# Optimization experiments

Hardware: AMD Instinct MI355X
Metric: run time of the kernel (lower is better)

## Reference

```python
import jax, jax.numpy as jnp
import numpy as np

EPS = 1e-5  # BatchNorm1d default eps


def _gcn_layer(x, src, dst, ew, W, b, N):
    # PyG GCNConv: h = x @ W, add self-loops (weight 1), symmetric norm, aggregate at dst, + bias
    h = x @ W
    loop = jnp.arange(N)
    src_a = jnp.concatenate([src, loop])
    dst_a = jnp.concatenate([dst, loop])
    ew_a = jnp.concatenate([ew, jnp.ones((N,), x.dtype)])
    deg = jax.ops.segment_sum(ew_a, dst_a, num_segments=N)  # [N]
    dinv = jax.lax.rsqrt(deg)  # deg >= 1 thanks to self-loops
    norm = dinv[src_a] * ew_a * dinv[dst_a]  # [E+N]
    out = jax.ops.segment_sum(h[src_a] * norm[:, None], dst_a, num_segments=N)
    return out + b


def _bn_relu(h, gamma, beta):
    # training-mode BatchNorm1d over the node dimension (biased variance)
    mean = h.mean(axis=0)
    var = jnp.mean((h - mean) ** 2, axis=0)
    return jax.nn.relu((h - mean) * jax.lax.rsqrt(var + EPS) * gamma + beta)


def setup_inputs() -> dict:
    key = jax.random.key(0)
    ks = jax.random.split(key, 8)
    N, E, D, H = 100000, 1600000, 64, 64
    x = jax.random.normal(ks[0], (N, D), dtype=jnp.float32)
    edge_index = jax.random.randint(ks[1], (2, E), 0, N, dtype=jnp.int64)
    edge_weight = jax.random.uniform(ks[2], (E,), dtype=jnp.float32)
    s = 1.0 / np.sqrt(D)
    W1 = jax.random.uniform(ks[3], (D, H), jnp.float32, -s, s)
    b1 = jnp.zeros((H,), jnp.float32)
    gamma1 = jnp.ones((H,), jnp.float32)
    beta1 = jnp.zeros((H,), jnp.float32)
    s2 = 1.0 / np.sqrt(H)
    W2 = jax.random.uniform(ks[4], (H, H), jnp.float32, -s2, s2)
    b2 = jnp.zeros((H,), jnp.float32)
    gamma2 = jnp.ones((H,), jnp.float32)
    beta2 = jnp.zeros((H,), jnp.float32)
    return {"x": x, "edge_index": edge_index, "edge_weight": edge_weight,
            "W1": W1, "b1": b1, "gamma1": gamma1, "beta1": beta1,
            "W2": W2, "b2": b2, "gamma2": gamma2, "beta2": beta2}


def reference(x, edge_index, edge_weight, W1, b1, gamma1, beta1, W2, b2, gamma2, beta2):
    N = x.shape[0]
    src, dst = edge_index[0], edge_index[1]  # messages flow src -> dst
    h = _gcn_layer(x, src, dst, edge_weight, W1, b1, N)
    h = _bn_relu(h, gamma1, beta1)
    h = _gcn_layer(h, src, dst, edge_weight, W2, b2, N)
    h = _bn_relu(h, gamma2, beta2)
    return h
```

## Files before the change

kernel.cpp:

```cpp
#include <hip/hip_runtime.h>
#include <hip/hip_fp16.h>


#define NPB   200
#define NBMAX 512
#define CAP   5120
#define CHUNK 8192

typedef unsigned long long u64;
typedef unsigned int u32;
typedef u32 u32x4 __attribute__((ext_vector_type(4)));

__global__ __launch_bounds__(512) void k_init(int* gcur, float* stats) {
  int t = threadIdx.x;
  if (t < NBMAX) gcur[t] = 0;
  if (t < 256) stats[t] = 0.f;
}

__global__ __launch_bounds__(256) void k_bucket(const int* __restrict__ ei,
                                                const float* __restrict__ ew,
                                                int* gcur, u64* __restrict__ bkt,
                                                int E, int NB) {
  __shared__ int lcnt[NBMAX];
  __shared__ int lbase[NBMAX];
  int t = threadIdx.x;
  for (int b = t; b < NBMAX; b += 256) lcnt[b] = 0;
  __syncthreads();
  int lo = blockIdx.x * CHUNK;
  int hi = min(lo + CHUNK, E);
  for (int i = lo + t; i < hi; i += 256)
    atomicAdd(&lcnt[ei[E + i] / NPB], 1);
  __syncthreads();
  for (int b = t; b < NB; b += 256) {
    int c = lcnt[b];
    lbase[b] = c ? atomicAdd(&gcur[b], c) : 0;
    lcnt[b] = 0;
  }
  __syncthreads();
  for (int i = lo + t; i < hi; i += 256) {
    int src = ei[i], dst = ei[E + i];
    float w = ew[i];
    int b = dst / NPB;
    int pos = lbase[b] + atomicAdd(&lcnt[b], 1);
    if (pos < CAP) {
      unsigned wq = (unsigned)(w * 1073741824.0f);
      if (wq > 0x3FFFFFFFu) wq = 0x3FFFFFFFu;
      bkt[(size_t)b * CAP + pos] =
          ((u64)(unsigned)dst << 47) | ((u64)(unsigned)src << 30) | (u64)wq;
    }
  }
}

__global__ __launch_bounds__(256) void k_sort(const u64* __restrict__ bkt,
                                              const int* __restrict__ gcur,
                                              u32* __restrict__ csr,
                                              int2* __restrict__ row,
                                              float* __restrict__ dinv, int N) {
  __shared__ u64 sorted[CAP];
  __shared__ int hist[256];
  __shared__ int offs[256];
  __shared__ int cur[NPB];
  __shared__ int cpArr[NPB];
  __shared__ float dv[NPB];
  int b = blockIdx.x, t = threadIdx.x;
  for (int i = t; i < CAP; i += 256) sorted[i] = 0ULL;
  hist[t] = 0;
  if (t < NPB) cur[t] = 0;
  __syncthreads();
  int cnt = min(gcur[b], CAP);
  size_t base = (size_t)b * CAP;
  for (int i = t; i < cnt; i += 256) {
    int dl = (int)(bkt[base + i] >> 47) - b * NPB;
    atomicAdd(&hist[dl], 1);
  }
  __syncthreads();
  int c = (t < NPB) ? ((hist[t] + 7) & ~7) : 0;
  offs[t] = c;
  __syncthreads();
  for (int o = 1; o < 256; o <<= 1) {
    int x = (t >= o) ? offs[t - o] : 0;
    __syncthreads();
    offs[t] += x;
    __syncthreads();
  }
  int total = offs[255];
  int myoff = offs[t] - c;
  __syncthreads();
  offs[t] = myoff;
  if (t < NPB) cpArr[t] = c;
  __syncthreads();
  for (int i = t; i < cnt; i += 256) {
    u64 u = bkt[base + i];
    int dl = (int)(u >> 47) - b * NPB;
    int pos = offs[dl] + atomicAdd(&cur[dl], 1);
    if (pos < CAP) sorted[pos] = u;
  }
  __syncthreads();
  for (int q = t; q < NPB * 4; q += 256) {
    int n = q >> 2, s = q & 3;
    int o = offs[n], cp = cpArr[n];
    float sum = 0.f;
    for (int j = o + s; j < o + cp; j += 4)
      sum += (float)(unsigned)(sorted[j] & 0x3FFFFFFFu);
    sum += __shfl_xor(sum, 1);
    sum += __shfl_xor(sum, 2);
    if (s == 0) {
      float d = rsqrtf(sum * (1.0f / 1073741824.0f) + 1.0f);
      dv[n] = d;
      int gn = b * NPB + n;
      if (gn < N) dinv[gn] = d;
    }
  }
  __syncthreads();
  int totalC = min(total, CAP);
  for (int j = t; j < totalC; j += 256) {
    u64 u = sorted[j];
    unsigned wq = (unsigned)(u & 0x3FFFFFFFu);
    int dl = (int)(u >> 47) - b * NPB;
    int dlc = (wq == 0) ? 0 : dl;
    float w = (float)wq * (1.0f / 1073741824.0f) * dv[dlc];
    unsigned q15 = (unsigned)(w * 32768.0f + 0.5f);
    if (q15 > 32767u) q15 = 32767u;
    unsigned s = (unsigned)((u >> 30) & 0x1FFFFu);
    csr[base + j] = (s << 15) | q15;
  }
  for (int n = t; n < NPB; n += 256) {
    int gn = b * NPB + n;
    if (gn < N) {
      int o = offs[n];
      int cp = min(cpArr[n], max(0, CAP - o)) & ~7;
      row[gn] = make_int2((int)(base + o), cp);
    }
  }
}

__global__ __launch_bounds__(256) void k_fold(u32* __restrict__ csr,
                                              const float* __restrict__ dinv,
                                              int total4, int N) {
  int i = blockIdx.x * 256 + threadIdx.x;
  if (i >= total4) return;
  uint4 q = ((uint4*)csr)[i];
#pragma unroll
  for (int k = 0; k < 4; ++k) {
    u32 u = (&q.x)[k];
    int s = (int)(u >> 15);
    float d = dinv[min(s, N - 1)];
    unsigned nq = (unsigned)((float)(u & 0x7FFFu) * d + 0.5f);
    (&q.x)[k] = (u & 0xFFFF8000u) | nq;
  }
  ((uint4*)csr)[i] = q;
}

__device__ inline unsigned pk2(float a, float b) {
  __half2 h = __floats2half2_rn(a, b);
  return *reinterpret_cast<unsigned*>(&h);
}

template <int FUSE>
__global__ __launch_bounds__(256) void k_gemm(const float* __restrict__ X,
                                              const float* __restrict__ W,
                                              __half* __restrict__ Y, int N,
                                              const float* __restrict__ scale,
                                              const float* __restrict__ shift) {
  __shared__ float Wl[64 * 64];
  __shared__ float sc[64], sh[64];
  int tid = threadIdx.x;
  {
    float4* Wl4 = (float4*)Wl;
    const float4* W4 = (const float4*)W;
#pragma unroll
    for (int i = 0; i < 4; ++i) Wl4[tid + i * 256] = W4[tid + i * 256];
  }
  if (FUSE && tid < 64) { sc[tid] = scale[tid]; sh[tid] = shift[tid]; }
  __syncthreads();
  int row = blockIdx.x * 64 + (tid >> 2);
  if (row >= N) return;
  int c0 = (tid & 3) * 16;
  float4 a0 = make_float4(0.f, 0.f, 0.f, 0.f), a1 = a0, a2 = a0, a3 = a0;
  const float4* Xr = (const float4*)(X + (size_t)row * 64);
#pragma unroll
  for (int kk = 0; kk < 16; ++kk) {
    float4 xv = Xr[kk];
    if (FUSE) {
      int k4 = kk * 4;
      xv.x = fmaxf(fmaf(xv.x, sc[k4 + 0], sh[k4 + 0]), 0.f);
      xv.y = fmaxf(fmaf(xv.y, sc[k4 + 1], sh[k4 + 1]), 0.f);
      xv.z = fmaxf(fmaf(xv.z, sc[k4 + 2], sh[k4 + 2]), 0.f);
      xv.w = fmaxf(fmaf(xv.w, sc[k4 + 3], sh[k4 + 3]), 0.f);
    }
    const float* wbase = &Wl[(kk * 4) * 64 + c0];
#pragma unroll
    for (int d = 0; d < 4; ++d) {
      float xk = (d == 0) ? xv.x : (d == 1) ? xv.y : (d == 2) ? xv.z : xv.w;
      const float4* Wr = (const float4*)(wbase + d * 64);
      float4 w0 = Wr[0], w1 = Wr[1], w2 = Wr[2], w3 = Wr[3];
      a0.x = fmaf(xk, w0.x, a0.x); a0.y = fmaf(xk, w0.y, a0.y);
      a0.z = fmaf(xk, w0.z, a0.z); a0.w = fmaf(xk, w0.w, a0.w);
      a1.x = fmaf(xk, w1.x, a1.x); a1.y = fmaf(xk, w1.y, a1.y);
      a1.z = fmaf(xk, w1.z, a1.z); a1.w = fmaf(xk, w1.w, a1.w);
      a2.x = fmaf(xk, w2.x, a2.x); a2.y = fmaf(xk, w2.y, a2.y);
      a2.z = fmaf(xk, w2.z, a2.z); a2.w = fmaf(xk, w2.w, a2.w);
      a3.x = fmaf(xk, w3.x, a3.x); a3.y = fmaf(xk, w3.y, a3.y);
      a3.z = fmaf(xk, w3.z, a3.z); a3.w = fmaf(xk, w3.w, a3.w);
    }
  }
  uint4 p0, p1;
  p0.x = pk2(a0.x, a0.y); p0.y = pk2(a0.z, a0.w);
  p0.z = pk2(a1.x, a1.y); p0.w = pk2(a1.z, a1.w);
  p1.x = pk2(a2.x, a2.y); p1.y = pk2(a2.z, a2.w);
  p1.z = pk2(a3.x, a3.y); p1.w = pk2(a3.z, a3.w);
  uint4* Y4 = (uint4*)(Y + (size_t)row * 64 + c0);
  Y4[0] = p0; Y4[1] = p1;
}

__global__ __launch_bounds__(256) void k_agg(const __half* __restrict__ H,
                                             const int2* __restrict__ row,
                                             const u32* __restrict__ csr,
                                             const float* __restrict__ dinv,
                                             const float* __restrict__ bias,
                                             float* __restrict__ out,
                                             float* __restrict__ sums,
                                             float* __restrict__ sumsq, int N) {
  const float QS = 1.0f / 32768.0f;
  int lane = threadIdx.x & 63;
  int wib = threadIdx.x >> 6;
  int wid = blockIdx.x * 4 + wib;
  int nw = gridDim.x * 4;
  float b = bias[lane];
  float ssum = 0.f, ssq = 0.f;
  for (int n = wid; n < N; n += nw) {
    int2 r = row[n];
    const u32x4* c4 = (const u32x4*)(csr + r.x);
    int cntp = r.y;
    float di = dinv[n];
    float hn = __half2float(H[(size_t)n * 64 + lane]);
    float acc0 = 0.f, acc1 = 0.f, acc2 = 0.f, acc3 = 0.f;
    for (int j = 0; j < cntp; j += 8) {
      u32x4 qa = __builtin_nontemporal_load(&c4[(j >> 2) + 0]);
      u32x4 qb = __builtin_nontemporal_load(&c4[(j >> 2) + 1]);
      int s0 = (int)(qa.x >> 15), s1 = (int)(qa.y >> 15);
      int s2 = (int)(qa.z >> 15), s3 = (int)(qa.w >> 15);
      int s4 = (int)(qb.x >> 15), s5 = (int)(qb.y >> 15);
      int s6 = (int)(qb.z >> 15), s7 = (int)(qb.w >> 15);
      float w0 = (float)(qa.x & 0x7FFFu) * QS, w1 = (float)(qa.y & 0x7FFFu) * QS;
      float w2 = (float)(qa.z & 0x7FFFu) * QS, w3 = (float)(qa.w & 0x7FFFu) * QS;
      float w4 = (float)(qb.x & 0x7FFFu) * QS, w5 = (float)(qb.y & 0x7FFFu) * QS;
      float w6 = (float)(qb.z & 0x7FFFu) * QS, w7 = (float)(qb.w & 0x7FFFu) * QS;
      float h0 = __half2float(H[(size_t)s0 * 64 + lane]);
      float h1 = __half2float(H[(size_t)s1 * 64 + lane]);
      float h2 = __half2float(H[(size_t)s2 * 64 + lane]);
      float h3 = __half2float(H[(size_t)s3 * 64 + lane]);
      float h4 = __half2float(H[(size_t)s4 * 64 + lane]);
      float h5 = __half2float(H[(size_t)s5 * 64 + lane]);
      float h6 = __half2float(H[(size_t)s6 * 64 + lane]);
      float h7 = __half2float(H[(size_t)s7 * 64 + lane]);
      acc0 = fmaf(w0, h0, acc0); acc1 = fmaf(w1, h1, acc1);
      acc2 = fmaf(w2, h2, acc2); acc3 = fmaf(w3, h3, acc3);
      acc0 = fmaf(w4, h4, acc0); acc1 = fmaf(w5, h5, acc1);
      acc2 = fmaf(w6, h6, acc2); acc3 = fmaf(w7, h7, acc3);
    }
    float v = (acc0 + acc1) + (acc2 + acc3) + di * di * hn + b;
    __builtin_nontemporal_store(v, &out[(size_t)n * 64 + lane]);
    ssum += v;
    ssq = fmaf(v, v, ssq);
  }
  __shared__ float ls[4][64];
  __shared__ float ls2[4][64];
  ls[wib][lane] = ssum; ls2[wib][lane] = ssq;
  __syncthreads();
  if (wib == 0) {
    float a = ls[0][lane] + ls[1][lane] + ls[2][lane] + ls[3][lane];
    float c = ls2[0][lane] + ls2[1][lane] + ls2[2][lane] + ls2[3][lane];
    atomicAdd(&sums[lane], a);
    atomicAdd(&sumsq[lane], c);
  }
}

__global__ __launch_bounds__(64) void k_finalize(const float* __restrict__ sums,
                                                 const float* __restrict__ sumsq,
                                                 const float* __restrict__ gamma,
                                                 const float* __restrict__ beta,
                                                 float* __restrict__ scale,
                                                 float* __restrict__ shift, float invN) {
  int t = threadIdx.x;
  if (t < 64) {
    float mean = sums[t] * invN;
    float var = sumsq[t] * invN - mean * mean;
    float sc = gamma[t] * rsqrtf(var + 1e-5f);
    scale[t] = sc;
    shift[t] = fmaf(-mean, sc, beta[t]);
  }
}

__global__ __launch_bounds__(256) void k_bnrelu(float* __restrict__ Y,
                                                const float* __restrict__ scale,
                                                const float* __restrict__ shift, int n4) {
  int i = blockIdx.x * 256 + threadIdx.x;
  if (i >= n4) return;
  float4 v = ((float4*)Y)[i];
  int f = (i & 15) * 4;
  v.x = fmaxf(fmaf(v.x, scale[f + 0], shift[f + 0]), 0.f);
  v.y = fmaxf(fmaf(v.y, scale[f + 1], shift[f + 1]), 0.f);
  v.z = fmaxf(fmaf(v.z, scale[f + 2], shift[f + 2]), 0.f);
  v.w = fmaxf(fmaf(v.w, scale[f + 3], shift[f + 3]), 0.f);
  ((float4*)Y)[i] = v;
}

extern "C" void kernel_launch(void* const* d_in, const int* in_sizes, int n_in,
                              void* d_out, int out_size, void* d_ws, size_t ws_size,
                              hipStream_t stream) {
  const float* x   = (const float*)d_in[0];
  const int*   ei  = (const int*)d_in[1];
  const float* ew  = (const float*)d_in[2];
  const float* W1  = (const float*)d_in[3];
  const float* b1  = (const float*)d_in[4];
  const float* g1  = (const float*)d_in[5];
  const float* be1 = (const float*)d_in[6];
  const float* W2  = (const float*)d_in[7];
  const float* b2  = (const float*)d_in[8];
  const float* g2  = (const float*)d_in[9];
  const float* be2 = (const float*)d_in[10];
  int N = in_sizes[0] / 64;
  int E = in_sizes[1] / 2;
  float* out = (float*)d_out;

  int NB = (N + NPB - 1) / NPB;

  char* ws = (char*)d_ws;
  size_t off = 0;
  auto alloc = [&](size_t bytes) {
    char* p = ws + off;
    off = (off + bytes + 255) & ~(size_t)255;
    return p;
  };

  int*    gcur  = (int*)alloc(NBMAX * 4);
  float*  dinv  = (float*)alloc((size_t)N * 4);
  __half* h1    = (__half*)alloc((size_t)N * 64 * 2);
  float*  stats = (float*)alloc(256 * 4);
  float*  scsh  = (float*)alloc(256 * 4);
  int2*   row   = (int2*)alloc((size_t)N * 8);
  u64*    bkt   = (u64*)alloc((size_t)NB * CAP * 8);
  u32*    csr   = (u32*)alloc((size_t)NB * CAP * 4);

  float *sums1 = stats, *sumsq1 = stats + 64, *sums2 = stats + 128, *sumsq2 = stats + 192;
  float *scale1 = scsh, *shift1 = scsh + 64, *scale2 = scsh + 128, *shift2 = scsh + 192;

  int total4 = NB * CAP / 4;

  k_init<<<1, 512, 0, stream>>>(gcur, stats);
  k_bucket<<<(E + CHUNK - 1) / CHUNK, 256, 0, stream>>>(ei, ew, gcur, bkt, E, NB);
  k_sort<<<NB, 256, 0, stream>>>(bkt, gcur, csr, row, dinv, N);
  k_fold<<<(total4 + 255) / 256, 256, 0, stream>>>(csr, dinv, total4, N);

  k_gemm<0><<<(N + 63) / 64, 256, 0, stream>>>(x, W1, h1, N, nullptr, nullptr);
  k_agg<<<2048, 256, 0, stream>>>(h1, row, csr, dinv, b1, out, sums1, sumsq1, N);
  k_finalize<<<1, 64, 0, stream>>>(sums1, sumsq1, g1, be1, scale1, shift1, 1.0f / N);

  k_gemm<1><<<(N + 63) / 64, 256, 0, stream>>>(out, W2, h1, N, scale1, shift1);
  k_agg<<<2048, 256, 0, stream>>>(h1, row, csr, dinv, b2, out, sums2, sumsq2, N);
  k_finalize<<<1, 64, 0, stream>>>(sums2, sumsq2, g2, be2, scale2, shift2, 1.0f / N);
  k_bnrelu<<<(N * 16 + 255) / 256, 256, 0, stream>>>(out, scale2, shift2, N * 16);
}
```

Before: 302.2 us.

## Split wave into two half-waves each gathering half2 features per edge

The aggregation kernel now has each 64-lane wave process two edges at once: lanes 0-31 and 32-63 each take alternating edges, and each lane loads a __half2 (two features) instead of a single half. The two half-wave partial sums are combined with a cross-lane shuffle before the store, and only the lower half writes output and stats. The aim is wider per-lane gather loads and fewer serial iterations per node. The grid size is also doubled. The cost is the extra shuffle and half-idle lanes at the epilogue.

Result: slower. 377.2 us (+24.8%).

```diff
diff --git a/kernel.cpp b/kernel.cpp
--- a/kernel.cpp
+++ b/kernel.cpp
@@ -10,6 +10,7 @@
 typedef unsigned long long u64;
 typedef unsigned int u32;
 typedef u32 u32x4 __attribute__((ext_vector_type(4)));
+typedef float f32x2 __attribute__((ext_vector_type(2)));
 
 __global__ __launch_bounds__(512) void k_init(int* gcur, float* stats) {
   int t = threadIdx.x;
@@ -222,51 +223,67 @@
                                              float* __restrict__ sums,
                                              float* __restrict__ sumsq, int N) {
   const float QS = 1.0f / 32768.0f;
+  const __half2* H2 = (const __half2*)H;
   int lane = threadIdx.x & 63;
   int wib = threadIdx.x >> 6;
+  int fp = lane & 31;
+  int hi = lane >> 5;
+  int f0 = fp * 2;
   int wid = blockIdx.x * 4 + wib;
   int nw = gridDim.x * 4;
-  float b = bias[lane];
-  float ssum = 0.f, ssq = 0.f;
+  float b0 = bias[f0], b1 = bias[f0 + 1];
+  float ssum0 = 0.f, ssq0 = 0.f, ssum1 = 0.f, ssq1 = 0.f;
   for (int n = wid; n < N; n += nw) {
     int2 r = row[n];
     const u32x4* c4 = (const u32x4*)(csr + r.x);
     int cntp = r.y;
     float di = dinv[n];
-    float hn = __half2float(H[(size_t)n * 64 + lane]);
-    float acc0 = 0.f, acc1 = 0.f, acc2 = 0.f, acc3 = 0.f;
+    float2 a0 = make_float2(0.f, 0.f), a1 = a0, a2 = a0, a3 = a0;
     for (int j = 0; j < cntp; j += 8) {
       u32x4 qa = __builtin_nontemporal_load(&c4[(j >> 2) + 0]);
       u32x4 qb = __builtin_nontemporal_load(&c4[(j >> 2) + 1]);
-      int s0 = (int)(qa.x >> 15), s1 = (int)(qa.y >> 15);
-      int s2 = (int)(qa.z >> 15), s3 = (int)(qa.w >> 15);
-      int s4 = (int)(qb.x >> 15), s5 = (int)(qb.y >> 15);
-      int s6 = (int)(qb.z >> 15), s7 = (int)(qb.w >> 15);
-      float w0 = (float)(qa.x & 0x7FFFu) * QS, w1 = (float)(qa.y & 0x7FFFu) * QS;
-      float w2 = (float)(qa.z & 0x7FFFu) * QS, w3 = (float)(qa.w & 0x7FFFu) * QS;
-      float w4 = (float)(qb.x & 0x7FFFu) * QS, w5 = (float)(qb.y & 0x7FFFu) * QS;
-      float w6 = (float)(qb.z & 0x7FFFu) * QS, w7 = (float)(qb.w & 0x7FFFu) * QS;
-      float h0 = __half2float(H[(size_t)s0 * 64 + lane]);
-      float h1 = __half2float(H[(size_t)s1 * 64 + lane]);
-      float h2 = __half2float(H[(size_t)s2 * 64 + lane]);
-      float h3 = __half2float(H[(size_t)s3 * 64 + lane]);
-      float h4 = __half2float(H[(size_t)s4 * 64 + lane]);
-      float h5 = __half2float(H[(size_t)s5 * 64 + lane]);
-      float h6 = __half2float(H[(size_t)s6 * 64 + lane]);
-      float h7 = __half2float(H[(size_t)s7 * 64 + lane]);
-      acc0 = fmaf(w0, h0, acc0); acc1 = fmaf(w1, h1, acc1);
-      acc2 = fmaf(w2, h2, acc2); acc3 = fmaf(w3, h3, acc3);
-      acc0 = fmaf(w4, h4, acc0); acc1 = fmaf(w5, h5, acc1);
-      acc2 = fmaf(w6, h6, acc2); acc3 = fmaf(w7, h7, acc3);
-    }
-    float v = (acc0 + acc1) + (acc2 + acc3) + di * di * hn + b;
-    __builtin_nontemporal_store(v, &out[(size_t)n * 64 + lane]);
-    ssum += v;
-    ssq = fmaf(v, v, ssq);
+      u32 e0 = hi ? qa.y : qa.x;
+      u32 e1 = hi ? qa.w : qa.z;
+      u32 e2 = hi ? qb.y : qb.x;
+      u32 e3 = hi ? qb.w : qb.z;
+      int s0 = (int)(e0 >> 15), s1 = (int)(e1 >> 15);
+      int s2 = (int)(e2 >> 15), s3 = (int)(e3 >> 15);
+      float w0 = (float)(e0 & 0x7FFFu) * QS;
+      float w1 = (float)(e1 & 0x7FFFu) * QS;
+      float w2 = (float)(e2 & 0x7FFFu) * QS;
+      float w3 = (float)(e3 & 0x7FFFu) * QS;
+      __half2 h0 = H2[(size_t)s0 * 32 + fp];
+      __half2 h1 = H2[(size_t)s1 * 32 + fp];
+      __half2 h2 = H2[(size_t)s2 * 32 + fp];
+      __half2 h3 = H2[(size_t)s3 * 32 + fp];
+      float2 g0 = __half22float2(h0), g1 = __half22float2(h1);
+      float2 g2 = __half22float2(h2), g3 = __half22float2(h3);
+      a0.x = fmaf(w0, g0.x, a0.x); a0.y = fmaf(w0, g0.y, a0.y);
+      a1.x = fmaf(w1, g1.x, a1.x); a1.y = fmaf(w1, g1.y, a1.y);
+      a2.x = fmaf(w2, g2.x, a2.x); a2.y = fmaf(w2, g2.y, a2.y);
+      a3.x = fmaf(w3, g3.x, a3.x); a3.y = fmaf(w3, g3.y, a3.y);
+    }
+    float ax = (a0.x + a1.x) + (a2.x + a3.x);
+    float ay = (a0.y + a1.y) + (a2.y + a3.y);
+    ax += __shfl_xor(ax, 32);
+    ay += __shfl_xor(ay, 32);
+    float2 hn = __half22float2(H2[(size_t)n * 32 + fp]);
+    float d2 = di * di;
+    float vx = ax + d2 * hn.x + b0;
+    float vy = ay + d2 * hn.y + b1;
+    if (lane < 32) {
+      f32x2 v2; v2.x = vx; v2.y = vy;
+      __builtin_nontemporal_store(v2, (f32x2*)&out[(size_t)n * 64 + f0]);
+    }
+    ssum0 += vx; ssq0 = fmaf(vx, vx, ssq0);
+    ssum1 += vy; ssq1 = fmaf(vy, vy, ssq1);
   }
   __shared__ float ls[4][64];
   __shared__ float ls2[4][64];
-  ls[wib][lane] = ssum; ls2[wib][lane] = ssq;
+  if (lane < 32) {
+    ls[wib][f0] = ssum0;  ls[wib][f0 + 1] = ssum1;
+    ls2[wib][f0] = ssq0;  ls2[wib][f0 + 1] = ssq1;
+  }
   __syncthreads();
   if (wib == 0) {
     float a = ls[0][lane] + ls[1][lane] + ls[2][lane] + ls[3][lane];
@@ -354,11 +371,11 @@
   k_fold<<<(total4 + 255) / 256, 256, 0, stream>>>(csr, dinv, total4, N);
 
   k_gemm<0><<<(N + 63) / 64, 256, 0, stream>>>(x, W1, h1, N, nullptr, nullptr);
-  k_agg<<<2048, 256, 0, stream>>>(h1, row, csr, dinv, b1, out, sums1, sumsq1, N);
+  k_agg<<<4096, 256, 0, stream>>>(h1, row, csr, dinv, b1, out, sums1, sumsq1, N);
   k_finalize<<<1, 64, 0, stream>>>(sums1, sumsq1, g1, be1, scale1, shift1, 1.0f / N);
 
   k_gemm<1><<<(N + 63) / 64, 256, 0, stream>>>(out, W2, h1, N, scale1, shift1);
-  k_agg<<<2048, 256, 0, stream>>>(h1, row, csr, dinv, b2, out, sums2, sumsq2, N);
+  k_agg<<<4096, 256, 0, stream>>>(h1, row, csr, dinv, b2, out, sums2, sumsq2, N);
   k_finalize<<<1, 64, 0, stream>>>(sums2, sumsq2, g2, be2, scale2, shift2, 1.0f / N);
   k_bnrelu<<<(N * 16 + 255) / 256, 256, 0, stream>>>(out, scale2, shift2, N * 16);
 }
```

## Compute degrees in separate pass, fold src norm into sort, fuse BN finalize

Applied to the files above, without the earlier changes.

Adds a k_deg kernel that computes dinv per bucket with integer shared atomics. This lets k_sort apply both the src and dst normalisation directly and drops the separate k_fold pass over the CSR. The BN finalize kernels are folded into the consumers (the second gemm and bnrelu), removing two tiny launches. The aggregation loop is unrolled to 16 edges per iteration with rows padded to multiples of 16, and CAP grows to fit the extra padding. The larger padding adds zero-weight work and raises shared memory use in k_sort, and the fixed-point integer degree sum loses some precision.

Measured after the change: 298.6 us. About the same (-1.2%).

```diff
diff --git a/kernel.cpp b/kernel.cpp
--- a/kernel.cpp
+++ b/kernel.cpp
@@ -4,7 +4,7 @@
 
 #define NPB   200
 #define NBMAX 512
-#define CAP   5120
+#define CAP   6144
 #define CHUNK 8192
 
 typedef unsigned long long u64;
@@ -51,11 +51,33 @@
   }
 }
 
+__global__ __launch_bounds__(256) void k_deg(const u64* __restrict__ bkt,
+                                             const int* __restrict__ gcur,
+                                             float* __restrict__ dinv, int N) {
+  __shared__ int dq[NPB];
+  int b = blockIdx.x, t = threadIdx.x;
+  for (int n = t; n < NPB; n += 256) dq[n] = 0;
+  __syncthreads();
+  int cnt = min(gcur[b], CAP);
+  size_t base = (size_t)b * CAP;
+  for (int i = t; i < cnt; i += 256) {
+    u64 u = bkt[base + i];
+    int dl = (int)(u >> 47) - b * NPB;
+    atomicAdd(&dq[dl], (int)((unsigned)(u & 0x3FFFFFFFu) >> 6));
+  }
+  __syncthreads();
+  for (int n = t; n < NPB; n += 256) {
+    int gn = b * NPB + n;
+    if (gn < N)
+      dinv[gn] = rsqrtf((float)dq[n] * (1.0f / 16777216.0f) + 1.0f);
+  }
+}
+
 __global__ __launch_bounds__(256) void k_sort(const u64* __restrict__ bkt,
                                               const int* __restrict__ gcur,
+                                              const float* __restrict__ dinv,
                                               u32* __restrict__ csr,
-                                              int2* __restrict__ row,
-                                              float* __restrict__ dinv, int N) {
+                                              int2* __restrict__ row, int N) {
   __shared__ u64 sorted[CAP];
   __shared__ int hist[256];
   __shared__ int offs[256];
@@ -65,7 +87,11 @@
   int b = blockIdx.x, t = threadIdx.x;
   for (int i = t; i < CAP; i += 256) sorted[i] = 0ULL;
   hist[t] = 0;
-  if (t < NPB) cur[t] = 0;
+  if (t < NPB) {
+    cur[t] = 0;
+    int gn = b * NPB + t;
+    dv[t] = (gn < N) ? dinv[gn] : 0.f;
+  }
   __syncthreads();
   int cnt = min(gcur[b], CAP);
   size_t base = (size_t)b * CAP;
@@ -74,7 +100,7 @@
     atomicAdd(&hist[dl], 1);
   }
   __syncthreads();
-  int c = (t < NPB) ? ((hist[t] + 7) & ~7) : 0;
+  int c = (t < NPB) ? ((hist[t] + 15) & ~15) : 0;
   offs[t] = c;
   __syncthreads();
   for (int o = 1; o < 256; o <<= 1) {
@@ -94,22 +120,6 @@
     int dl = (int)(u >> 47) - b * NPB;
     int pos = offs[dl] + atomicAdd(&cur[dl], 1);
     if (pos < CAP) sorted[pos] = u;
-  }
-  __syncthreads();
-  for (int q = t; q < NPB * 4; q += 256) {
-    int n = q >> 2, s = q & 3;
-    int o = offs[n], cp = cpArr[n];
-    float sum = 0.f;
-    for (int j = o + s; j < o + cp; j += 4)
-      sum += (float)(unsigned)(sorted[j] & 0x3FFFFFFFu);
-    sum += __shfl_xor(sum, 1);
-    sum += __shfl_xor(sum, 2);
-    if (s == 0) {
-      float d = rsqrtf(sum * (1.0f / 1073741824.0f) + 1.0f);
-      dv[n] = d;
-      int gn = b * NPB + n;
-      if (gn < N) dinv[gn] = d;
-    }
   }
   __syncthreads();
   int totalC = min(total, CAP);
@@ -118,37 +128,20 @@
     unsigned wq = (unsigned)(u & 0x3FFFFFFFu);
     int dl = (int)(u >> 47) - b * NPB;
     int dlc = (wq == 0) ? 0 : dl;
-    float w = (float)wq * (1.0f / 1073741824.0f) * dv[dlc];
+    unsigned s = (unsigned)((u >> 30) & 0x1FFFFu);
+    float w = (float)wq * (1.0f / 1073741824.0f) * dv[dlc] * dinv[s];
     unsigned q15 = (unsigned)(w * 32768.0f + 0.5f);
     if (q15 > 32767u) q15 = 32767u;
-    unsigned s = (unsigned)((u >> 30) & 0x1FFFFu);
     csr[base + j] = (s << 15) | q15;
   }
   for (int n = t; n < NPB; n += 256) {
     int gn = b * NPB + n;
     if (gn < N) {
       int o = offs[n];
-      int cp = min(cpArr[n], max(0, CAP - o)) & ~7;
+      int cp = min(cpArr[n], max(0, CAP - o)) & ~15;
       row[gn] = make_int2((int)(base + o), cp);
     }
   }
-}
-
-__global__ __launch_bounds__(256) void k_fold(u32* __restrict__ csr,
-                                              const float* __restrict__ dinv,
-                                              int total4, int N) {
-  int i = blockIdx.x * 256 + threadIdx.x;
-  if (i >= total4) return;
-  uint4 q = ((uint4*)csr)[i];
-#pragma unroll
-  for (int k = 0; k < 4; ++k) {
-    u32 u = (&q.x)[k];
-    int s = (int)(u >> 15);
-    float d = dinv[min(s, N - 1)];
-    unsigned nq = (unsigned)((float)(u & 0x7FFFu) * d + 0.5f);
-    (&q.x)[k] = (u & 0xFFFF8000u) | nq;
-  }
-  ((uint4*)csr)[i] = q;
 }
 
 __device__ inline unsigned pk2(float a, float b) {
@@ -160,8 +153,11 @@
 __global__ __launch_bounds__(256) void k_gemm(const float* __restrict__ X,
                                               const float* __restrict__ W,
                                               __half* __restrict__ Y, int N,
-                                              const float* __restrict__ scale,
-                                              const float* __restrict__ shift) {
+                                              const float* __restrict__ sums,
+                                              const float* __restrict__ sumsq,
+                                              const float* __restrict__ gamma,
+                                              const float* __restrict__ beta,
+                                              float invN) {
   __shared__ float Wl[64 * 64];
   __shared__ float sc[64], sh[64];
   int tid = threadIdx.x;
@@ -171,7 +167,13 @@
 #pragma unroll
     for (int i = 0; i < 4; ++i) Wl4[tid + i * 256] = W4[tid + i * 256];
   }
-  if (FUSE && tid < 64) { sc[tid] = scale[tid]; sh[tid] = shift[tid]; }
+  if (FUSE && tid < 64) {
+    float mean = sums[tid] * invN;
+    float var = sumsq[tid] * invN - mean * mean;
+    float s = gamma[tid] * rsqrtf(var + 1e-5f);
+    sc[tid] = s;
+    sh[tid] = fmaf(-mean, s, beta[tid]);
+  }
   __syncthreads();
   int row = blockIdx.x * 64 + (tid >> 2);
   if (row >= N) return;
@@ -235,17 +237,19 @@
     float di = dinv[n];
     float hn = __half2float(H[(size_t)n * 64 + lane]);
     float acc0 = 0.f, acc1 = 0.f, acc2 = 0.f, acc3 = 0.f;
-    for (int j = 0; j < cntp; j += 8) {
+    for (int j = 0; j < cntp; j += 16) {
       u32x4 qa = __builtin_nontemporal_load(&c4[(j >> 2) + 0]);
       u32x4 qb = __builtin_nontemporal_load(&c4[(j >> 2) + 1]);
+      u32x4 qc = __builtin_nontemporal_load(&c4[(j >> 2) + 2]);
+      u32x4 qd = __builtin_nontemporal_load(&c4[(j >> 2) + 3]);
       int s0 = (int)(qa.x >> 15), s1 = (int)(qa.y >> 15);
       int s2 = (int)(qa.z >> 15), s3 = (int)(qa.w >> 15);
       int s4 = (int)(qb.x >> 15), s5 = (int)(qb.y >> 15);
       int s6 = (int)(qb.z >> 15), s7 = (int)(qb.w >> 15);
-      float w0 = (float)(qa.x & 0x7FFFu) * QS, w1 = (float)(qa.y & 0x7FFFu) * QS;
-      float w2 = (float)(qa.z & 0x7FFFu) * QS, w3 = (float)(qa.w & 0x7FFFu) * QS;
-      float w4 = (float)(qb.x & 0x7FFFu) * QS, w5 = (float)(qb.y & 0x7FFFu) * QS;
-      float w6 = (float)(qb.z & 0x7FFFu) * QS, w7 = (float)(qb.w & 0x7FFFu) * QS;
+      int s8 = (int)(qc.x >> 15), s9 = (int)(qc.y >> 15);
+      int sa = (int)(qc.z >> 15), sb = (int)(qc.w >> 15);
+      int sc = (int)(qd.x >> 15), sd = (int)(qd.y >> 15);
+      int se = (int)(qd.z >> 15), sf = (int)(qd.w >> 15);
       float h0 = __half2float(H[(size_t)s0 * 64 + lane]);
       float h1 = __half2float(H[(size_t)s1 * 64 + lane]);
       float h2 = __half2float(H[(size_t)s2 * 64 + lane]);
@@ -254,10 +258,30 @@
       float h5 = __half2float(H[(size_t)s5 * 64 + lane]);
       float h6 = __half2float(H[(size_t)s6 * 64 + lane]);
       float h7 = __half2float(H[(size_t)s7 * 64 + lane]);
-      acc0 = fmaf(w0, h0, acc0); acc1 = fmaf(w1, h1, acc1);
-      acc2 = fmaf(w2, h2, acc2); acc3 = fmaf(w3, h3, acc3);
-      acc0 = fmaf(w4, h4, acc0); acc1 = fmaf(w5, h5, acc1);
-      acc2 = fmaf(w6, h6, acc2); acc3 = fmaf(w7, h7, acc3);
+      float h8 = __half2float(H[(size_t)s8 * 64 + lane]);
+      float h9 = __half2float(H[(size_t)s9 * 64 + lane]);
+      float ha = __half2float(H[(size_t)sa * 64 + lane]);
+      float hb = __half2float(H[(size_t)sb * 64 + lane]);
+      float hc = __half2float(H[(size_t)sc * 64 + lane]);
+      float hd = __half2float(H[(size_t)sd * 64 + lane]);
+      float he = __half2float(H[(size_t)se * 64 + lane]);
+      float hf = __half2float(H[(size_t)sf * 64 + lane]);
+      acc0 = fmaf((float)(qa.x & 0x7FFFu) * QS, h0, acc0);
+      acc1 = fmaf((float)(qa.y & 0x7FFFu) * QS, h1, acc1);
+      acc2 = fmaf((float)(qa.z & 0x7FFFu) * QS, h2, acc2);
+      acc3 = fmaf((float)(qa.w & 0x7FFFu) * QS, h3, acc3);
+      acc0 = fmaf((float)(qb.x & 0x7FFFu) * QS, h4, acc0);
+      acc1 = fmaf((float)(qb.y & 0x7FFFu) * QS, h5, acc1);
+      acc2 = fmaf((float)(qb.z & 0x7FFFu) * QS, h6, acc2);
+      acc3 = fmaf((float)(qb.w & 0x7FFFu) * QS, h7, acc3);
+      acc0 = fmaf((float)(qc.x & 0x7FFFu) * QS, h8, acc0);
+      acc1 = fmaf((float)(qc.y & 0x7FFFu) * QS, h9, acc1);
+      acc2 = fmaf((float)(qc.z & 0x7FFFu) * QS, ha, acc2);
+      acc3 = fmaf((float)(qc.w & 0x7FFFu) * QS, hb, acc3);
+      acc0 = fmaf((float)(qd.x & 0x7FFFu) * QS, hc, acc0);
+      acc1 = fmaf((float)(qd.y & 0x7FFFu) * QS, hd, acc1);
+      acc2 = fmaf((float)(qd.z & 0x7FFFu) * QS, he, acc2);
+      acc3 = fmaf((float)(qd.w & 0x7FFFu) * QS, hf, acc3);
     }
     float v = (acc0 + acc1) + (acc2 + acc3) + di * di * hn + b;
     __builtin_nontemporal_store(v, &out[(size_t)n * 64 + lane]);
@@ -276,33 +300,30 @@
   }
 }
 
-__global__ __launch_bounds__(64) void k_finalize(const float* __restrict__ sums,
-                                                 const float* __restrict__ sumsq,
-                                                 const float* __restrict__ gamma,
-                                                 const float* __restrict__ beta,
-                                                 float* __restrict__ scale,
-                                                 float* __restrict__ shift, float invN) {
-  int t = threadIdx.x;
-  if (t < 64) {
-    float mean = sums[t] * invN;
-    float var = sumsq[t] * invN - mean * mean;
-    float sc = gamma[t] * rsqrtf(var + 1e-5f);
-    scale[t] = sc;
-    shift[t] = fmaf(-mean, sc, beta[t]);
-  }
-}
-
 __global__ __launch_bounds__(256) void k_bnrelu(float* __restrict__ Y,
-                                                const float* __restrict__ scale,
-                                                const float* __restrict__ shift, int n4) {
-  int i = blockIdx.x * 256 + threadIdx.x;
+                                                const float* __restrict__ sums,
+                                                const float* __restrict__ sumsq,
+                                                const float* __restrict__ gamma,
+                                                const float* __restrict__ beta,
+                                                float invN, int n4) {
+  __shared__ float sc[64], sh[64];
+  int tid = threadIdx.x;
+  if (tid < 64) {
+    float mean = sums[tid] * invN;
+    float var = sumsq[tid] * invN - mean * mean;
+    float s = gamma[tid] * rsqrtf(var + 1e-5f);
+    sc[tid] = s;
+    sh[tid] = fmaf(-mean, s, beta[tid]);
+  }
+  __syncthreads();
+  int i = blockIdx.x * 256 + tid;
   if (i >= n4) return;
   float4 v = ((float4*)Y)[i];
   int f = (i & 15) * 4;
-  v.x = fmaxf(fmaf(v.x, scale[f + 0], shift[f + 0]), 0.f);
-  v.y = fmaxf(fmaf(v.y, scale[f + 1], shift[f + 1]), 0.f);
-  v.z = fmaxf(fmaf(v.z, scale[f + 2], shift[f + 2]), 0.f);
-  v.w = fmaxf(fmaf(v.w, scale[f + 3], shift[f + 3]), 0.f);
+  v.x = fmaxf(fmaf(v.x, sc[f + 0], sh[f + 0]), 0.f);
+  v.y = fmaxf(fmaf(v.y, sc[f + 1], sh[f + 1]), 0.f);
+  v.z = fmaxf(fmaf(v.z, sc[f + 2], sh[f + 2]), 0.f);
+  v.w = fmaxf(fmaf(v.w, sc[f + 3], sh[f + 3]), 0.f);
   ((float4*)Y)[i] = v;
 }
 
@@ -338,27 +359,25 @@
   float*  dinv  = (float*)alloc((size_t)N * 4);
   __half* h1    = (__half*)alloc((size_t)N * 64 * 2);
   float*  stats = (float*)alloc(256 * 4);
-  float*  scsh  = (float*)alloc(256 * 4);
   int2*   row   = (int2*)alloc((size_t)N * 8);
   u64*    bkt   = (u64*)alloc((size_t)NB * CAP * 8);
   u32*    csr   = (u32*)alloc((size_t)NB * CAP * 4);
 
   float *sums1 = stats, *sumsq1 = stats + 64, *sums2 = stats + 128, *sumsq2 = stats + 192;
-  float *scale1 = scsh, *shift1 = scsh + 64, *scale2 = scsh + 128, *shift2 = scsh + 192;
-
-  int total4 = NB * CAP / 4;
+  float invN = 1.0f / N;
 
   k_init<<<1, 512, 0, stream>>>(gcur, stats);
   k_bucket<<<(E + CHUNK - 1) / CHUNK, 256, 0, stream>>>(ei, ew, gcur, bkt, E, NB);
-  k_sort<<<NB, 256, 0, stream>>>(bkt, gcur, csr, row, dinv, N);
-  k_fold<<<(total4 + 255) / 256, 256, 0, stream>>>(csr, dinv, total4, N);
-
-  k_gemm<0><<<(N + 63) / 64, 256, 0, stream>>>(x, W1, h1, N, nullptr, nullptr);
+  k_deg<<<NB, 256, 0, stream>>>(bkt, gcur, dinv, N);
+  k_sort<<<NB, 256, 0, stream>>>(bkt, gcur, dinv, csr, row, N);
+
+  k_gemm<0><<<(N + 63) / 64, 256, 0, stream>>>(x, W1, h1, N, nullptr, nullptr,
+                                               nullptr, nullptr, 0.f);
   k_agg<<<2048, 256, 0, stream>>>(h1, row, csr, dinv, b1, out, sums1, sumsq1, N);
-  k_finalize<<<1, 64, 0, stream>>>(sums1, sumsq1, g1, be1, scale1, shift1, 1.0f / N);
-
-  k_gemm<1><<<(N + 63) / 64, 256, 0, stream>>>(out, W2, h1, N, scale1, shift1);
+
+  k_gemm<1><<<(N + 63) / 64, 256, 0, stream>>>(out, W2, h1, N, sums1, sumsq1,
+                                               g1, be1, invN);
   k_agg<<<2048, 256, 0, stream>>>(h1, row, csr, dinv, b2, out, sums2, sumsq2, N);
-  k_finalize<<<1, 64, 0, stream>>>(sums2, sumsq2, g2, be2, scale2, shift2, 1.0f / N);
-  k_bnrelu<<<(N * 16 + 255) / 256, 256, 0, stream>>>(out, scale2, shift2, N * 16);
-}
+  k_bnrelu<<<(N * 16 + 255) / 256, 256, 0, stream>>>(out, sums2, sumsq2, g2, be2,
+                                                     invN, N * 16);
+}
```
